# Performance work log

Measured on AMD Instinct MI355X. Metric: run time of the kernel, lower is better.

The kernel has to match this reference:

```python
import jax, jax.numpy as jnp
import numpy as np

# Intrinsics from innerProdLoss defaults
FX, FY, CX, CY = 48.0, 48.0, 48.0, 36.0
H, W = int(2 * CY), int(2 * CX)  # 72, 96
N = H * W                         # 6912 pixels
SIGMA2 = 1.0                      # geometric Gaussian-kernel bandwidth (reconstructed kern_mat)
EPS = 1e-8


def make_yz1_grid():
    # K = [[cx,fx,0],[cy,0,fy],[1,0,0]]; yz1_grid = inv(K) @ uv1_grid, shape [3, N]
    K = np.array([[CX, FX, 0.0], [CY, 0.0, FY], [1.0, 0.0, 0.0]], dtype=np.float64)
    invK = np.linalg.inv(K).astype(np.float32)
    u = np.arange(W, dtype=np.float32)
    v = np.arange(H, dtype=np.float32)
    uu = np.tile(u[None, :], (H, 1)).reshape(-1)
    vv = np.tile(v[:, None], (1, W)).reshape(-1)
    uv1 = np.stack([uu, vv, np.ones_like(uu)], axis=0)  # [3, N]
    return jnp.asarray(invK @ uv1)

YZ1 = make_yz1_grid()  # [3, N]


def kern_mat(p1, p2):
    # p1, p2: [B, 3, N] point clouds -> [B, N, N] Gaussian kernel exp(-||d||^2 / (2 sigma^2)).
    # Squared distances via norms + cross term (no [B,3,N,N] diff tensor).
    n1 = jnp.sum(p1 * p1, axis=1)                    # [B, N]
    n2 = jnp.sum(p2 * p2, axis=1)                    # [B, N]
    cross = jnp.einsum('bcm,bcn->bmn', p1, p2)       # [B, N, N]
    d2 = jnp.maximum(n1[:, :, None] + n2[:, None, :] - 2.0 * cross, 0.0)
    return jnp.exp(-d2 / (2.0 * SIGMA2))


def gramian(f1, f2):
    # f1, f2: [B, C, H, W] -> gramian [B, N, N] of L2-normalized features (norm_mode=1, kernalize=False).
    B, C, Hh, Ww = f1.shape
    n = Hh * Ww
    f1 = f1.reshape(B, C, n)
    f2 = f2.reshape(B, C, n)
    norm1 = jnp.linalg.norm(f1, axis=1)              # [B, N]
    norm2 = jnp.linalg.norm(f2, axis=1)
    fea_norm_sum = jnp.sum(norm1) + jnp.sum(norm2)
    f1n = f1 / (norm1[:, None, :] + EPS)
    f2n = f2 / (norm2[:, None, :] + EPS)
    gram = jnp.einsum('bcm,bcn->bmn', f1n, f2n) / n  # norm_mode=1 normalization
    return gram, fea_norm_sum


def setup_inputs() -> dict:
    key = jax.random.key(0)
    k1, k2, k3, k4, k5 = jax.random.split(key, 5)
    B, C = 1, 16
    feature1 = jax.random.normal(k1, (B, C, H, W), jnp.float32)
    feature2 = jax.random.normal(k2, (B, C, H, W), jnp.float32)
    depth1 = jax.random.uniform(k3, (B, 1, H, W), jnp.float32, 0.5, 5.0)
    depth2 = jax.random.uniform(k4, (B, 1, H, W), jnp.float32, 0.5, 5.0)
    pose1_2 = jnp.tile(jnp.eye(4, dtype=jnp.float32)[None], (B, 1, 1))
    pose_noise = jnp.eye(4, dtype=jnp.float32) + 0.01 * jax.random.normal(k5, (4, 4), jnp.float32)
    return {"feature1": feature1, "feature2": feature2, "depth1": depth1,
            "depth2": depth2, "pose1_2": pose1_2, "pose_noise": pose_noise}


def reference(feature1, feature2, depth1, depth2, pose1_2, pose_noise):
    B = depth1.shape[0]
    # gen_3D: back-project pixels using depth
    xyz1 = YZ1[None] * depth1.reshape(B, 1, N)       # [B, 3, N]
    xyz2 = YZ1[None] * depth2.reshape(B, 1, N)
    xyz2_homo = jnp.concatenate([xyz2, jnp.ones((B, 1, N), xyz2.dtype)], axis=1)  # [B, 4, N]
    xyz2_trans = jnp.matmul(pose1_2, xyz2_homo)[:, :3, :]

    gram_feat, fea_norm_sum = gramian(feature1, feature2)
    pcl_diff_exp = kern_mat(xyz1, xyz2_trans)

    # L2_norm=True, diff_mode=True -> scale by 100
    fea_norm_sum = fea_norm_sum * 100.0

    # diff_mode: noisy pose branch
    pose_noisy = jnp.matmul(pose1_2, pose_noise)
    xyz2_trans_noisy = jnp.matmul(pose_noisy, xyz2_homo)[:, :3, :]
    pcl_diff_exp_noisy = kern_mat(xyz1, xyz2_trans_noisy)

    inner_neg = -jnp.sum((pcl_diff_exp - pcl_diff_exp_noisy) * gram_feat)
    final_loss = inner_neg  # sparse_mode=False
    return final_loss, inner_neg, fea_norm_sum
```

## Files before the change

kernel.cpp:

```cpp
#include <hip/hip_runtime.h>
#include <math.h>

#define NPIX 6912
#define LOG2E 1.4426950408889634f

typedef __fp16 v8h  __attribute__((ext_vector_type(8)));
typedef float  v16f __attribute__((ext_vector_type(16)));

#define OFF_ROWFEAT 0
#define OFF_ROWGEO  221184
#define OFF_COLFEAT 442368
#define OFF_COLB1   663552
#define OFF_COLB2   884736

__device__ __forceinline__ float fast_exp2(float x) { return __builtin_amdgcn_exp2f(x); }

__device__ __forceinline__ float wave_reduce_64(float v) {
    #pragma unroll
    for (int o = 32; o > 0; o >>= 1) v += __shfl_down(v, o, 64);
    return v;
}

__device__ __forceinline__ void split_hl(float x, __fp16& h, __fp16& l) {
    h = (__fp16)x;
    l = (__fp16)(x - (float)h);
}

__global__ __launch_bounds__(64)
void preproc_kernel(const float* __restrict__ f1, const float* __restrict__ f2,
                    const float* __restrict__ d1, const float* __restrict__ d2,
                    const float* __restrict__ pose, const float* __restrict__ pnz,
                    char* __restrict__ wsb, float* __restrict__ out) {
    const int i = blockIdx.x * 64 + threadIdx.x;

    __fp16* rowfeat = (__fp16*)(wsb + OFF_ROWFEAT);
    __fp16* rowgeo  = (__fp16*)(wsb + OFF_ROWGEO);
    __fp16* colfeat = (__fp16*)(wsb + OFF_COLFEAT);
    __fp16* colB1   = (__fp16*)(wsb + OFF_COLB1);
    __fp16* colB2   = (__fp16*)(wsb + OFF_COLB2);

    float P[12];
    #pragma unroll
    for (int k = 0; k < 12; k++) P[k] = pose[k];
    float Q[12];
    #pragma unroll
    for (int r = 0; r < 3; r++) {
        #pragma unroll
        for (int c = 0; c < 4; c++) {
            float s = 0.0f;
            #pragma unroll
            for (int k = 0; k < 4; k++) s = fmaf(pose[r * 4 + k], pnz[k * 4 + c], s);
            Q[r * 4 + c] = s;
        }
    }

    const float inv48 = 1.0f / 48.0f;
    const int u = i % 96;
    const int v = i / 96;
    const float y1 = fmaf((float)u, inv48, -1.0f);
    const float y2 = fmaf((float)v, inv48, -0.75f);

    const float dep1 = d1[i];
    const float px = dep1, py = y1 * dep1, pz = y2 * dep1;
    const float n1 = px * px + py * py + pz * pz;
    const float wlog = -0.5f * LOG2E * n1;

    const float ptx = LOG2E * px, pty = LOG2E * py, ptz = LOG2E * pz;
    __fp16 phx, phy, phz, plx, ply, plz, wh, wl;
    split_hl(ptx, phx, plx);
    split_hl(pty, phy, ply);
    split_hl(ptz, phz, plz);
    split_hl(wlog, wh, wl);
    {
        __fp16 rg[16] = {phx, phy, phz,  phx, phy, phz,  plx, ply, plz,
                         (__fp16)1.0f, (__fp16)1.0f, wh, wl,
                         (__fp16)0, (__fp16)0, (__fp16)0};
        *(v8h*)(rowgeo + (size_t)i * 16)     = *(v8h*)(rg);
        *(v8h*)(rowgeo + (size_t)i * 16 + 8) = *(v8h*)(rg + 8);
    }

    const float dep2 = d2[i];
    const float a = dep2, b = y1 * dep2, g = y2 * dep2;
    const float t0 = P[0] * a + P[1] * b + P[2]  * g + P[3];
    const float t1 = P[4] * a + P[5] * b + P[6]  * g + P[7];
    const float t2 = P[8] * a + P[9] * b + P[10] * g + P[11];
    const float q0 = Q[0] * a + Q[1] * b + Q[2]  * g + Q[3];
    const float q1 = Q[4] * a + Q[5] * b + Q[6]  * g + Q[7];
    const float q2 = Q[8] * a + Q[9] * b + Q[10] * g + Q[11];
    const float nt = t0 * t0 + t1 * t1 + t2 * t2;
    const float nq = q0 * q0 + q1 * q1 + q2 * q2;
    const float cA = -0.5f * LOG2E * nt;
    const float dc = 0.5f * LOG2E * (nt - nq);

    __fp16 thx, thy, thz, tlx, tly, tlz, cAh, cAl, dch, dcl;
    split_hl(t0, thx, tlx);
    split_hl(t1, thy, tly);
    split_hl(t2, thz, tlz);
    split_hl(cA, cAh, cAl);
    split_hl(dc, dch, dcl);
    {
        __fp16 b1a[16] = {thx, thy, thz,  tlx, tly, tlz,  thx, thy, thz,
                          cAh, cAl, (__fp16)1.0f, (__fp16)1.0f,
                          (__fp16)0, (__fp16)0, (__fp16)0};
        *(v8h*)(colB1 + (size_t)i * 16)     = *(v8h*)(b1a);
        *(v8h*)(colB1 + (size_t)i * 16 + 8) = *(v8h*)(b1a + 8);
    }
    const __fp16 dtx = (__fp16)(q0 - t0), dty = (__fp16)(q1 - t1), dtz = (__fp16)(q2 - t2);
    {
        __fp16 b2a[16] = {dtx, dty, dtz,  (__fp16)0, (__fp16)0, (__fp16)0,  dtx, dty, dtz,
                          dch, dcl, (__fp16)0, (__fp16)0,
                          (__fp16)0, (__fp16)0, (__fp16)0};
        *(v8h*)(colB2 + (size_t)i * 16)     = *(v8h*)(b2a);
        *(v8h*)(colB2 + (size_t)i * 16 + 8) = *(v8h*)(b2a + 8);
    }

    float s1 = 0.0f, s2 = 0.0f;
    float v1[16], v2[16];
    #pragma unroll
    for (int cc = 0; cc < 16; cc++) {
        v1[cc] = f1[cc * NPIX + i];
        v2[cc] = f2[cc * NPIX + i];
        s1 = fmaf(v1[cc], v1[cc], s1);
        s2 = fmaf(v2[cc], v2[cc], s2);
    }
    const float nrm1 = sqrtf(s1), nrm2 = sqrtf(s2);
    const float r1 = 1.0f / (nrm1 + 1e-8f), r2 = 1.0f / (nrm2 + 1e-8f);
    {
        __fp16 rf[16], cf[16];
        #pragma unroll
        for (int cc = 0; cc < 16; cc++) {
            rf[cc] = (__fp16)(v1[cc] * r1);
            cf[cc] = (__fp16)(v2[cc] * r2);
        }
        *(v8h*)(rowfeat + (size_t)i * 16)     = *(v8h*)(rf);
        *(v8h*)(rowfeat + (size_t)i * 16 + 8) = *(v8h*)(rf + 8);
        *(v8h*)(colfeat + (size_t)i * 16)     = *(v8h*)(cf);
        *(v8h*)(colfeat + (size_t)i * 16 + 8) = *(v8h*)(cf + 8);
    }

    float tot = wave_reduce_64(nrm1 + nrm2);
    if (threadIdx.x == 0) atomicAdd(out + 2, 100.0f * tot);
}

__global__ __launch_bounds__(256)
void pair_kernel(const char* __restrict__ wsb, float* __restrict__ out) {
    __shared__ float smem4[4];

    const __fp16* rowfeat = (const __fp16*)(wsb + OFF_ROWFEAT);
    const __fp16* rowgeo  = (const __fp16*)(wsb + OFF_ROWGEO);
    const __fp16* colfeat = (const __fp16*)(wsb + OFF_COLFEAT);
    const __fp16* colB1   = (const __fp16*)(wsb + OFF_COLB1);
    const __fp16* colB2   = (const __fp16*)(wsb + OFF_COLB2);

    const int t = threadIdx.x;
    const int w = t >> 6;
    const int L = t & 63;
    const int c31 = L & 31;
    const int kh8 = (L >> 5) * 8;

    v8h afeat[2], ageo[2];
    #pragma unroll
    for (int s = 0; s < 2; s++) {
        const int arow = blockIdx.y * 256 + w * 64 + s * 32 + c31;
        afeat[s] = *(const v8h*)(rowfeat + (size_t)arow * 16 + kh8);
        ageo[s]  = *(const v8h*)(rowgeo  + (size_t)arow * 16 + kh8);
    }

    const int cbase = blockIdx.x * 192;
    const size_t boff0 = (size_t)(cbase + c31) * 16 + kh8;

    float acc = 0.0f;
    v8h bf = *(const v8h*)(colfeat + boff0);
    v8h b1 = *(const v8h*)(colB1   + boff0);
    v8h b2 = *(const v8h*)(colB2   + boff0);

    #pragma unroll
    for (int ct = 0; ct < 6; ct++) {
        v8h nbf, nb1, nb2;
        if (ct < 5) {
            const size_t noff = boff0 + (size_t)(ct + 1) * 32 * 16;
            nbf = *(const v8h*)(colfeat + noff);
            nb1 = *(const v8h*)(colB1   + noff);
            nb2 = *(const v8h*)(colB2   + noff);
        }

        v16f z = {};
        #pragma unroll
        for (int s = 0; s < 2; s++) {
            const v16f dotv = __builtin_amdgcn_mfma_f32_32x32x16_f16(afeat[s], bf, z, 0, 0, 0);
            const v16f a1v  = __builtin_amdgcn_mfma_f32_32x32x16_f16(ageo[s],  b1, z, 0, 0, 0);
            const v16f dlv  = __builtin_amdgcn_mfma_f32_32x32x16_f16(ageo[s],  b2, z, 0, 0, 0);
            #pragma unroll
            for (int i = 0; i < 16; i++) {
                const float e1 = fast_exp2(a1v[i]);
                const float e2 = fast_exp2(a1v[i] + dlv[i]);
                acc = fmaf(e1 - e2, dotv[i], acc);
            }
        }
        if (ct < 5) { bf = nbf; b1 = nb1; b2 = nb2; }
    }

    float v = wave_reduce_64(acc);
    if (L == 0) smem4[w] = v;
    __syncthreads();
    if (t == 0) {
        const float tot = smem4[0] + smem4[1] + smem4[2] + smem4[3];
        const float vc = -tot * (1.0f / (float)NPIX);
        atomicAdd(out + 0, vc);
        atomicAdd(out + 1, vc);
    }
}

extern "C" void kernel_launch(void* const* d_in, const int* in_sizes, int n_in,
                              void* d_out, int out_size, void* d_ws, size_t ws_size,
                              hipStream_t stream) {
    const float* feature1 = (const float*)d_in[0];
    const float* feature2 = (const float*)d_in[1];
    const float* depth1   = (const float*)d_in[2];
    const float* depth2   = (const float*)d_in[3];
    const float* pose1_2  = (const float*)d_in[4];
    const float* posenz   = (const float*)d_in[5];
    float* out = (float*)d_out;
    char*  wsb = (char*)d_ws;

    (void)hipMemsetAsync(d_out, 0, (size_t)out_size * sizeof(float), stream);

    preproc_kernel<<<108, 64, 0, stream>>>(feature1, feature2, depth1, depth2,
                                           pose1_2, posenz, wsb, out);
    dim3 grid(36, 27);
    pair_kernel<<<grid, 256, 0, stream>>>(wsb, out);
}
```

Before: 101.0 us.

## Retile pair kernel and replace atomics with partial-sum finalize kernel

Each wave now covers 32 rows against 288 columns, where before it covered 64 rows against 192 columns, giving a 24x54 grid of 1296 blocks instead of 972. The exp loop is split into two independent accumulators. The memset and float atomics are replaced by per-block partial sums written to workspace and reduced deterministically in a single-block finalize kernel. This adds a third kernel launch in exchange for removing the memset, the atomic contention and a per-wave row dependency.

Result: faster. 85.90 us (-14.9%).

```diff
diff --git a/kernel.cpp b/kernel.cpp
--- a/kernel.cpp
+++ b/kernel.cpp
@@ -12,6 +12,10 @@
 #define OFF_COLFEAT 442368
 #define OFF_COLB1   663552
 #define OFF_COLB2   884736
+#define OFF_PART    1105920
+#define OFF_NPART   1111104
+#define NPART_BLOCKS 1296
+#define NNORM_BLOCKS 108
 
 __device__ __forceinline__ float fast_exp2(float x) { return __builtin_amdgcn_exp2f(x); }
 
@@ -19,6 +23,18 @@
     #pragma unroll
     for (int o = 32; o > 0; o >>= 1) v += __shfl_down(v, o, 64);
     return v;
+}
+
+__device__ __forceinline__ float block_reduce_256(float v, float* smem4) {
+    __syncthreads();
+    v = wave_reduce_64(v);
+    const int lane = threadIdx.x & 63;
+    const int w = threadIdx.x >> 6;
+    if (lane == 0) smem4[w] = v;
+    __syncthreads();
+    float r = 0.0f;
+    if (threadIdx.x == 0) r = smem4[0] + smem4[1] + smem4[2] + smem4[3];
+    return r;
 }
 
 __device__ __forceinline__ void split_hl(float x, __fp16& h, __fp16& l) {
@@ -30,7 +46,7 @@
 void preproc_kernel(const float* __restrict__ f1, const float* __restrict__ f2,
                     const float* __restrict__ d1, const float* __restrict__ d2,
                     const float* __restrict__ pose, const float* __restrict__ pnz,
-                    char* __restrict__ wsb, float* __restrict__ out) {
+                    char* __restrict__ wsb) {
     const int i = blockIdx.x * 64 + threadIdx.x;
 
     __fp16* rowfeat = (__fp16*)(wsb + OFF_ROWFEAT);
@@ -38,6 +54,7 @@
     __fp16* colfeat = (__fp16*)(wsb + OFF_COLFEAT);
     __fp16* colB1   = (__fp16*)(wsb + OFF_COLB1);
     __fp16* colB2   = (__fp16*)(wsb + OFF_COLB2);
+    float*  npart   = (float*)(wsb + OFF_NPART);
 
     float P[12];
     #pragma unroll
@@ -139,11 +156,11 @@
     }
 
     float tot = wave_reduce_64(nrm1 + nrm2);
-    if (threadIdx.x == 0) atomicAdd(out + 2, 100.0f * tot);
+    if (threadIdx.x == 0) npart[blockIdx.x] = tot;
 }
 
 __global__ __launch_bounds__(256)
-void pair_kernel(const char* __restrict__ wsb, float* __restrict__ out) {
+void pair_kernel(const char* __restrict__ wsb) {
     __shared__ float smem4[4];
 
     const __fp16* rowfeat = (const __fp16*)(wsb + OFF_ROWFEAT);
@@ -151,6 +168,7 @@
     const __fp16* colfeat = (const __fp16*)(wsb + OFF_COLFEAT);
     const __fp16* colB1   = (const __fp16*)(wsb + OFF_COLB1);
     const __fp16* colB2   = (const __fp16*)(wsb + OFF_COLB2);
+    float*        part    = (float*)(const_cast<char*>(wsb) + OFF_PART);
 
     const int t = threadIdx.x;
     const int w = t >> 6;
@@ -158,26 +176,22 @@
     const int c31 = L & 31;
     const int kh8 = (L >> 5) * 8;
 
-    v8h afeat[2], ageo[2];
-    #pragma unroll
-    for (int s = 0; s < 2; s++) {
-        const int arow = blockIdx.y * 256 + w * 64 + s * 32 + c31;
-        afeat[s] = *(const v8h*)(rowfeat + (size_t)arow * 16 + kh8);
-        ageo[s]  = *(const v8h*)(rowgeo  + (size_t)arow * 16 + kh8);
-    }
-
-    const int cbase = blockIdx.x * 192;
+    const int arow = blockIdx.y * 128 + w * 32 + c31;
+    const v8h afeat = *(const v8h*)(rowfeat + (size_t)arow * 16 + kh8);
+    const v8h ageo  = *(const v8h*)(rowgeo  + (size_t)arow * 16 + kh8);
+
+    const int cbase = blockIdx.x * 288;
     const size_t boff0 = (size_t)(cbase + c31) * 16 + kh8;
 
-    float acc = 0.0f;
+    float acc0 = 0.0f, acc1 = 0.0f;
     v8h bf = *(const v8h*)(colfeat + boff0);
     v8h b1 = *(const v8h*)(colB1   + boff0);
     v8h b2 = *(const v8h*)(colB2   + boff0);
 
     #pragma unroll
-    for (int ct = 0; ct < 6; ct++) {
+    for (int ct = 0; ct < 9; ct++) {
         v8h nbf, nb1, nb2;
-        if (ct < 5) {
+        if (ct < 8) {
             const size_t noff = boff0 + (size_t)(ct + 1) * 32 * 16;
             nbf = *(const v8h*)(colfeat + noff);
             nb1 = *(const v8h*)(colB1   + noff);
@@ -185,29 +199,48 @@
         }
 
         v16f z = {};
+        const v16f dotv = __builtin_amdgcn_mfma_f32_32x32x16_f16(afeat, bf, z, 0, 0, 0);
+        const v16f a1v  = __builtin_amdgcn_mfma_f32_32x32x16_f16(ageo,  b1, z, 0, 0, 0);
+        const v16f dlv  = __builtin_amdgcn_mfma_f32_32x32x16_f16(ageo,  b2, z, 0, 0, 0);
+
         #pragma unroll
-        for (int s = 0; s < 2; s++) {
-            const v16f dotv = __builtin_amdgcn_mfma_f32_32x32x16_f16(afeat[s], bf, z, 0, 0, 0);
-            const v16f a1v  = __builtin_amdgcn_mfma_f32_32x32x16_f16(ageo[s],  b1, z, 0, 0, 0);
-            const v16f dlv  = __builtin_amdgcn_mfma_f32_32x32x16_f16(ageo[s],  b2, z, 0, 0, 0);
-            #pragma unroll
-            for (int i = 0; i < 16; i++) {
-                const float e1 = fast_exp2(a1v[i]);
-                const float e2 = fast_exp2(a1v[i] + dlv[i]);
-                acc = fmaf(e1 - e2, dotv[i], acc);
-            }
-        }
-        if (ct < 5) { bf = nbf; b1 = nb1; b2 = nb2; }
-    }
-
-    float v = wave_reduce_64(acc);
+        for (int i = 0; i < 8; i++) {
+            const float e1a = fast_exp2(a1v[i]);
+            const float e2a = fast_exp2(a1v[i] + dlv[i]);
+            const float e1b = fast_exp2(a1v[i + 8]);
+            const float e2b = fast_exp2(a1v[i + 8] + dlv[i + 8]);
+            acc0 = fmaf(e1a - e2a, dotv[i], acc0);
+            acc1 = fmaf(e1b - e2b, dotv[i + 8], acc1);
+        }
+        if (ct < 8) { bf = nbf; b1 = nb1; b2 = nb2; }
+    }
+
+    float v = wave_reduce_64(acc0 + acc1);
     if (L == 0) smem4[w] = v;
     __syncthreads();
+    if (t == 0)
+        part[blockIdx.y * 24 + blockIdx.x] = smem4[0] + smem4[1] + smem4[2] + smem4[3];
+}
+
+__global__ __launch_bounds__(256)
+void finalize_kernel(const char* __restrict__ wsb, float* __restrict__ out) {
+    __shared__ float smem4[4];
+    const float* part  = (const float*)(wsb + OFF_PART);
+    const float* npart = (const float*)(wsb + OFF_NPART);
+    const int t = threadIdx.x;
+
+    float s = 0.0f;
+    for (int i = t; i < NPART_BLOCKS; i += 256) s += part[i];
+    const float tot = block_reduce_256(s, smem4);
+
+    float ns = (t < NNORM_BLOCKS) ? npart[t] : 0.0f;
+    const float ntot = block_reduce_256(ns, smem4);
+
     if (t == 0) {
-        const float tot = smem4[0] + smem4[1] + smem4[2] + smem4[3];
         const float vc = -tot * (1.0f / (float)NPIX);
-        atomicAdd(out + 0, vc);
-        atomicAdd(out + 1, vc);
+        out[0] = vc;
+        out[1] = vc;
+        out[2] = 100.0f * ntot;
     }
 }
 
@@ -223,10 +256,9 @@
     float* out = (float*)d_out;
     char*  wsb = (char*)d_ws;
 
-    (void)hipMemsetAsync(d_out, 0, (size_t)out_size * sizeof(float), stream);
-
     preproc_kernel<<<108, 64, 0, stream>>>(feature1, feature2, depth1, depth2,
-                                           pose1_2, posenz, wsb, out);
-    dim3 grid(36, 27);
-    pair_kernel<<<grid, 256, 0, stream>>>(wsb, out);
-}
+                                           pose1_2, posenz, wsb);
+    dim3 grid(24, 54);
+    pair_kernel<<<grid, 256, 0, stream>>>(wsb);
+    finalize_kernel<<<1, 256, 0, stream>>>(wsb, out);
+}
```
